# Kernel tuning notes

Hardware: AMD Instinct MI355X
Metric: run time of the kernel (lower is better)

The kernel has to match this reference:

```python
import jax, jax.numpy as jnp
import numpy as np

B, T, H, C = 256, 784, 512, 10
TRUNC = 100


def setup_inputs() -> dict:
    key = jax.random.key(0)
    ks = jax.random.split(key, 11)
    s_in = 1.0  # xavier-ish scales
    def init(k, shape, fan_in):
        return jax.random.normal(k, shape, dtype=jnp.float32) * (1.0 / np.sqrt(fan_in))
    return {
        "x": jax.random.normal(ks[0], (B, T), dtype=jnp.float32),
        "W_ih1": init(ks[1], (4 * H, 1), 1),
        "W_hh1": init(ks[2], (4 * H, H), H),
        "b_ih1": jnp.zeros((4 * H,), dtype=jnp.float32),
        "b_hh1": jnp.zeros((4 * H,), dtype=jnp.float32),
        "W_ih2": init(ks[3], (4 * H, H), H),
        "W_hh2": init(ks[4], (4 * H, H), H),
        "b_ih2": jnp.zeros((4 * H,), dtype=jnp.float32),
        "b_hh2": jnp.zeros((4 * H,), dtype=jnp.float32),
        "W_fc": init(ks[5], (C, H), H),
        "b_fc": jnp.zeros((C,), dtype=jnp.float32),
    }


def _lstm_cell(pre, h, c, W_hh, b_hh):
    # pre: input projection [B,4H]; PyTorch LSTMCell gate order: i, f, g, o
    gates = pre + h @ W_hh.T + b_hh
    i, f, g, o = jnp.split(gates, 4, axis=-1)
    c_new = jax.nn.sigmoid(f) * c + jax.nn.sigmoid(i) * jnp.tanh(g)
    h_new = jax.nn.sigmoid(o) * jnp.tanh(c_new)
    return h_new, c_new


def _forward(x, W_ih1, W_hh1, b_ih1, b_hh1, W_ih2, W_hh2, b_ih2, b_hh2, W_fc, b_fc):
    # Precompute input projections for layer 1 across all timesteps: x is scalar per step.
    # pre1_all: [T, B, 4H]
    pre1_all = x.T[:, :, None] * W_ih1[:, 0][None, None, :] + b_ih1
    t_idx = jnp.arange(T)

    def step(carry, xs):
        h1, c1, h2, c2 = carry
        pre1, t = xs
        # truncation point (detach) is identity in forward; kept for structure
        stop = (t % TRUNC) == 0
        sg = lambda a: jnp.where(stop, jax.lax.stop_gradient(a), a)
        h1, c1, h2, c2 = sg(h1), sg(c1), sg(h2), sg(c2)
        h1, c1 = _lstm_cell(pre1, h1, c1, W_hh1, b_hh1)
        pre2 = c1 @ W_ih2.T + b_ih2  # layer 2 consumes layer-1 CELL state
        h2, c2 = _lstm_cell(pre2, h2, c2, W_hh2, b_hh2)
        return (h1, c1, h2, c2), h2

    z = jnp.zeros((B, H), dtype=x.dtype)
    _, outs = jax.lax.scan(step, (z, z, z, z), (pre1_all, t_idx))  # outs: [T,B,H]
    outs = outs.transpose(1, 0, 2)  # [B,T,H]
    out = outs @ W_fc.T + b_fc  # [B,T,C]
    return out


def reference(x, W_ih1, W_hh1, b_ih1, b_hh1, W_ih2, W_hh2, b_ih2, b_hh2, W_fc, b_fc):
    return _forward(x, W_ih1, W_hh1, b_ih1, b_hh1, W_ih2, W_hh2, b_ih2, b_hh2, W_fc, b_fc)
```

## Files before the change

### kernel.cpp

```cpp
#include <hip/hip_runtime.h>


constexpr int Bn = 256;
constexpr int Tn = 784;
constexpr int Hn = 512;
constexpr int Cn = 10;

typedef short s16x8 __attribute__((ext_vector_type(8)));
typedef float f32x4 __attribute__((ext_vector_type(4)));

__device__ __forceinline__ unsigned short f2bf(float f) {
  unsigned u = __float_as_uint(f);
  u += 0x7FFFu + ((u >> 16) & 1u);
  return (unsigned short)(u >> 16);
}
__device__ __forceinline__ float bf2f(unsigned short s) {
  return __uint_as_float(((unsigned)s) << 16);
}
__device__ __forceinline__ float sigm(float v) { return 1.f / (1.f + __expf(-v)); }
__device__ __forceinline__ float tanh_(float v) {
  float vc = fminf(fmaxf(v, -15.f), 15.f);
  float e = __expf(2.f * vc);
  return (e - 1.f) / (e + 1.f);
}

__device__ __forceinline__ s16x8 load16_l2(const unsigned short* p) {
  s16x8 r;
  asm volatile("global_load_dwordx4 %0, %1, off sc0"
               : "=v"(r) : "v"(p) : "memory");
  return r;
}
__device__ __forceinline__ void store2_l2(unsigned short* p, unsigned short v) {
  unsigned w = v;
  asm volatile("global_store_short %0, %1, off"
               :: "v"(p), "v"(w) : "memory");
}
__device__ __forceinline__ void vm0_fence() {
  asm volatile("s_waitcnt vmcnt(0)" ::: "memory");
  __builtin_amdgcn_sched_barrier(0);
}
__device__ __forceinline__ unsigned ld_flag(const unsigned* p) {
  unsigned r;
  asm volatile("global_load_dword %0, %1, off sc0 sc1\n\ts_waitcnt vmcnt(0)"
               : "=v"(r) : "v"(p) : "memory");
  return r;
}

__device__ __forceinline__ void stage_w(char* smem, const float* W0,
                                        int js, int tid, int base) {
  for (int idx = tid * 4; idx < 64 * 512; idx += 1024) {
    int row = idx >> 9, kk = idx & 511;
    int n = ((row >> 4) << 9) + js + (row & 15);
    float4 w = *(const float4*)(W0 + (size_t)n * Hn + kk);
    short4 v = { (short)f2bf(w.x), (short)f2bf(w.y), (short)f2bf(w.z), (short)f2bf(w.w) };
    int byte = base + (row << 10) + ((((kk >> 3) ^ (row & 7)) << 4)) + ((kk & 7) << 1);
    *(short4*)(smem + byte) = v;
  }
}

__global__ void __launch_bounds__(256, 1)
lstm2_kernel(const float* __restrict__ x,
             const float* __restrict__ W_ih1, const float* __restrict__ W_hh1,
             const float* __restrict__ b_ih1, const float* __restrict__ b_hh1,
             const float* __restrict__ W_ih2, const float* __restrict__ W_hh2,
             const float* __restrict__ b_ih2, const float* __restrict__ b_hh2,
             const float* __restrict__ W_fc, const float* __restrict__ b_fc,
             float* __restrict__ out,
             unsigned* __restrict__ cnts,
             unsigned short* __restrict__ h1b,
             unsigned short* __restrict__ c1b,
             unsigned short* __restrict__ h2b)
{
  extern __shared__ char smem[];
  const int tid = threadIdx.x;
  const int wv = tid >> 6;
  const int l = tid & 63;

  if (tid == 0) {
    unsigned xcc;
    asm volatile("s_getreg_b32 %0, hwreg(HW_REG_XCC_ID)" : "=s"(xcc));
    xcc &= 7u;
    unsigned rk = atomicAdd(&cnts[512 + xcc * 16], 1u);
    *(unsigned*)(smem + 131064) = xcc;
    *(unsigned*)(smem + 131060) = rk;
  }
  __syncthreads();
  const int s8   = (int)*(const unsigned*)(smem + 131064);
  const int rank = (int)(*(const unsigned*)(smem + 131060) & 31u);
  const int rb = s8 << 5;
  const int js = rank << 4;
  unsigned* cnt = cnts + s8 * 64;

  const int rA = l & 15, lg = l >> 4, lx = l & 7;
  const bool isW1 = (wv < 2);

  s16x8 bw[64];
  stage_w(smem, W_hh1, js, tid, 0);
  __syncthreads();
  if (isW1) {
#pragma unroll
    for (int g = 0; g < 4; ++g)
#pragma unroll
      for (int kc = 0; kc < 16; ++kc)
        bw[(g << 4) + kc] =
            *(const s16x8*)(smem + (((g << 4) + rA) << 10) + ((((kc << 2) + lg) ^ lx) << 4));
  }
  __syncthreads();
  stage_w(smem, W_hh2, js, tid, 0);
  __syncthreads();
  if (!isW1) {
#pragma unroll
    for (int g = 0; g < 4; ++g)
#pragma unroll
      for (int kc = 0; kc < 16; ++kc)
        bw[(g << 4) + kc] =
            *(const s16x8*)(smem + (((g << 4) + rA) << 10) + ((((kc << 2) + lg) ^ lx) << 4));
  }
  __syncthreads();
  stage_w(smem, W_ih2, js, tid, 0);
  {
    unsigned short* wf = (unsigned short*)(smem + 65536);
    for (int idx = tid; idx < Cn * Hn; idx += 256) wf[idx] = f2bf(W_fc[idx]);
    if (tid < Cn) ((float*)(smem + 65536 + Cn * Hn * 2))[tid] = b_fc[tid];
  }
  __syncthreads();

  float wih1g[4], bg[4];
  {
    int col = js + rA;
#pragma unroll
    for (int g = 0; g < 4; ++g) {
      int n = (g << 9) + col;
      if (isW1) { wih1g[g] = W_ih1[n]; bg[g] = b_ih1[n] + b_hh1[n]; }
      else      { wih1g[g] = 0.f;      bg[g] = b_ih2[n] + b_hh2[n]; }
    }
  }

  const int rf = isW1 ? wv : (wv - 2);
  const int arow  = rb + (rf << 4) + rA;
  const int myrow = rb + (rf << 4) + (lg << 2);
  const int colj = js + rA;
  const int bfc = rb + rank;
  const int cg = wv * 5;

  const size_t SLAB = (size_t)Bn * Hn;
  float cst[4] = {0.f, 0.f, 0.f, 0.f};

  for (int k = 0; k <= Tn + 1; ++k) {
    if (tid == 0 && k > 0) {
      int g = 0;
      for (;;) {
        unsigned a = ld_flag(cnt);
        if ((int)a >= (k << 5)) break;
        if (++g > (1 << 20)) break;
        __builtin_amdgcn_s_sleep(1);
      }
    }
    __syncthreads();

    s16x8 h8;
    if (isW1 && k >= 2)
      h8 = load16_l2(h2b + (size_t)(k & 1) * SLAB + (size_t)bfc * Hn + (l << 3));

    if (isW1) {
      if (k < Tn) {
        float xv[4];
#pragma unroll
        for (int r = 0; r < 4; ++r) xv[r] = x[(size_t)(myrow + r) * Tn + k];
        s16x8 af[16];
        const unsigned short* Ab =
            h1b + (size_t)((k - 1) & 1) * SLAB + (size_t)arow * Hn + (lg << 3);
#pragma unroll
        for (int kc = 0; kc < 16; ++kc) af[kc] = load16_l2(Ab + kc * 32);
        vm0_fence();
        f32x4 acc[4];
#pragma unroll
        for (int g = 0; g < 4; ++g) acc[g] = f32x4{0.f, 0.f, 0.f, 0.f};
#pragma unroll
        for (int kc = 0; kc < 16; ++kc)
#pragma unroll
          for (int g = 0; g < 4; ++g)
            acc[g] = __builtin_amdgcn_mfma_f32_16x16x32_bf16(af[kc], bw[(g << 4) + kc], acc[g], 0, 0, 0);
        unsigned short* h1w = h1b + (size_t)(k & 1) * SLAB;
        unsigned short* c1w = c1b + (size_t)(k & 1) * SLAB;
#pragma unroll
        for (int r = 0; r < 4; ++r) {
          float iv = sigm(acc[0][r] + xv[r] * wih1g[0] + bg[0]);
          float ff = sigm(acc[1][r] + xv[r] * wih1g[1] + bg[1]);
          float gv = tanh_(acc[2][r] + xv[r] * wih1g[2] + bg[2]);
          float ov = sigm(acc[3][r] + xv[r] * wih1g[3] + bg[3]);
          float c = ff * cst[r] + iv * gv;
          cst[r] = c;
          float h = ov * tanh_(c);
          size_t off = (size_t)(myrow + r) * Hn + colj;
          store2_l2(h1w + off, f2bf(h));
          store2_l2(c1w + off, f2bf(c));
        }
      }
    } else {
      if (k >= 1 && k <= Tn) {
        const int t = k - 1;
        s16x8 af[16], cf[16];
        const unsigned short* Ab =
            h2b + (size_t)((t - 1) & 1) * SLAB + (size_t)arow * Hn + (lg << 3);
        const unsigned short* Cb =
            c1b + (size_t)(t & 1) * SLAB + (size_t)arow * Hn + (lg << 3);
#pragma unroll
        for (int kc = 0; kc < 16; ++kc) af[kc] = load16_l2(Ab + kc * 32);
#pragma unroll
        for (int kc = 0; kc < 16; ++kc) cf[kc] = load16_l2(Cb + kc * 32);
        vm0_fence();
        f32x4 acc[4];
#pragma unroll
        for (int g = 0; g < 4; ++g) acc[g] = f32x4{0.f, 0.f, 0.f, 0.f};
#pragma unroll
        for (int kc = 0; kc < 16; ++kc)
#pragma unroll
          for (int g = 0; g < 4; ++g)
            acc[g] = __builtin_amdgcn_mfma_f32_16x16x32_bf16(af[kc], bw[(g << 4) + kc], acc[g], 0, 0, 0);
#pragma unroll
        for (int kc = 0; kc < 16; ++kc)
#pragma unroll
          for (int g = 0; g < 4; ++g) {
            int byte = (((g << 4) + rA) << 10) + ((((kc << 2) + lg) ^ lx) << 4);
            acc[g] = __builtin_amdgcn_mfma_f32_16x16x32_bf16(cf[kc], *(const s16x8*)(smem + byte), acc[g], 0, 0, 0);
          }
        unsigned short* h2w = h2b + (size_t)(t & 1) * SLAB;
#pragma unroll
        for (int r = 0; r < 4; ++r) {
          float iv = sigm(acc[0][r] + bg[0]);
          float ff = sigm(acc[1][r] + bg[1]);
          float gv = tanh_(acc[2][r] + bg[2]);
          float ov = sigm(acc[3][r] + bg[3]);
          float c = ff * cst[r] + iv * gv;
          cst[r] = c;
          float h = ov * tanh_(c);
          store2_l2(h2w + (size_t)(myrow + r) * Hn + colj, f2bf(h));
        }
      }
    }

    vm0_fence();
    __syncthreads();
    if (tid == 0) atomicAdd(cnt, 1u);

    if (isW1 && k >= 2) {
      const unsigned short* wf = (const unsigned short*)(smem + 65536);
      float rs[5];
#pragma unroll
      for (int c5 = 0; c5 < 5; ++c5) {
        s16x8 w8 = *(const s16x8*)(wf + (size_t)(cg + c5) * Hn + (l << 3));
        float sum = 0.f;
#pragma unroll
        for (int i = 0; i < 8; ++i)
          sum += bf2f((unsigned short)h8[i]) * bf2f((unsigned short)w8[i]);
        rs[c5] = sum;
      }
#pragma unroll
      for (int c5 = 0; c5 < 5; ++c5) {
#pragma unroll
        for (int off = 32; off > 0; off >>= 1)
          rs[c5] += __shfl_xor(rs[c5], off);
      }
      if (l < 5) {
        float v = (l == 0) ? rs[0] : (l == 1) ? rs[1] : (l == 2) ? rs[2] : (l == 3) ? rs[3] : rs[4];
        v += ((const float*)(smem + 65536 + Cn * Hn * 2))[cg + l];
        out[(size_t)bfc * (Tn * Cn) + (size_t)(k - 2) * Cn + (cg + l)] = v;
      }
    }
  }
}

extern "C" void kernel_launch(void* const* d_in, const int* in_sizes, int n_in,
                              void* d_out, int out_size, void* d_ws, size_t ws_size,
                              hipStream_t stream) {
  const float* x     = (const float*)d_in[0];
  const float* W_ih1 = (const float*)d_in[1];
  const float* W_hh1 = (const float*)d_in[2];
  const float* b_ih1 = (const float*)d_in[3];
  const float* b_hh1 = (const float*)d_in[4];
  const float* W_ih2 = (const float*)d_in[5];
  const float* W_hh2 = (const float*)d_in[6];
  const float* b_ih2 = (const float*)d_in[7];
  const float* b_hh2 = (const float*)d_in[8];
  const float* W_fc  = (const float*)d_in[9];
  const float* b_fc  = (const float*)d_in[10];
  float* out = (float*)d_out;

  unsigned* cnts = (unsigned*)d_ws;
  unsigned short* h1b = (unsigned short*)((char*)d_ws + 4096);
  unsigned short* c1b = h1b + (size_t)2 * Bn * Hn;
  unsigned short* h2b = c1b + (size_t)2 * Bn * Hn;

  size_t zbytes = 4096 + (size_t)3 * 2 * Bn * Hn * sizeof(unsigned short);
  hipMemsetAsync(d_ws, 0, zbytes, stream);

  (void)hipFuncSetAttribute((const void*)lstm2_kernel,
                            hipFuncAttributeMaxDynamicSharedMemorySize, 131072);

  lstm2_kernel<<<dim3(256), dim3(256), 131072, stream>>>(
      x, W_ih1, W_hh1, b_ih1, b_hh1, W_ih2, W_hh2, b_ih2, b_hh2, W_fc, b_fc,
      out, cnts, h1b, c1b, h2b);
}
```

Baseline: 5.399 ms.

## Replace atomic step counter with per-block flags polled by a full wavefront

Each block now publishes its step number with a plain system-coherent store to its own flag slot instead of atomically incrementing a shared per-group counter. Wave 0 polls all 32 flags in parallel and uses a wave vote to detect completion. Separately, the per-fragment loads are merged into one inline-asm block of 16 immediate-offset loads, the four scalar stores are merged into one asm block with immediate offsets, and per-buffer base pointers are precomputed. The aim is to cut atomic contention and address arithmetic on the per-timestep critical path, at the cost of a wider workspace and a heavier polling wave.

```diff
diff --git a/kernel.cpp b/kernel.cpp
--- a/kernel.cpp
+++ b/kernel.cpp
@@ -30,20 +30,52 @@
                : "=v"(r) : "v"(p) : "memory");
   return r;
 }
-__device__ __forceinline__ void store2_l2(unsigned short* p, unsigned short v) {
-  unsigned w = v;
-  asm volatile("global_store_short %0, %1, off"
-               :: "v"(p), "v"(w) : "memory");
+__device__ __forceinline__ void load16x16_l2(const unsigned short* p, s16x8* f) {
+  asm volatile(
+      "global_load_dwordx4 %0, %16, off sc0\n\t"
+      "global_load_dwordx4 %1, %16, off offset:64 sc0\n\t"
+      "global_load_dwordx4 %2, %16, off offset:128 sc0\n\t"
+      "global_load_dwordx4 %3, %16, off offset:192 sc0\n\t"
+      "global_load_dwordx4 %4, %16, off offset:256 sc0\n\t"
+      "global_load_dwordx4 %5, %16, off offset:320 sc0\n\t"
+      "global_load_dwordx4 %6, %16, off offset:384 sc0\n\t"
+      "global_load_dwordx4 %7, %16, off offset:448 sc0\n\t"
+      "global_load_dwordx4 %8, %16, off offset:512 sc0\n\t"
+      "global_load_dwordx4 %9, %16, off offset:576 sc0\n\t"
+      "global_load_dwordx4 %10, %16, off offset:640 sc0\n\t"
+      "global_load_dwordx4 %11, %16, off offset:704 sc0\n\t"
+      "global_load_dwordx4 %12, %16, off offset:768 sc0\n\t"
+      "global_load_dwordx4 %13, %16, off offset:832 sc0\n\t"
+      "global_load_dwordx4 %14, %16, off offset:896 sc0\n\t"
+      "global_load_dwordx4 %15, %16, off offset:960 sc0"
+      : "=&v"(f[0]), "=&v"(f[1]), "=&v"(f[2]), "=&v"(f[3]),
+        "=&v"(f[4]), "=&v"(f[5]), "=&v"(f[6]), "=&v"(f[7]),
+        "=&v"(f[8]), "=&v"(f[9]), "=&v"(f[10]), "=&v"(f[11]),
+        "=&v"(f[12]), "=&v"(f[13]), "=&v"(f[14]), "=&v"(f[15])
+      : "v"(p) : "memory");
+}
+__device__ __forceinline__ void store4_l2(unsigned short* p, unsigned v0,
+                                          unsigned v1, unsigned v2, unsigned v3) {
+  asm volatile(
+      "global_store_short %0, %1, off\n\t"
+      "global_store_short %0, %2, off offset:1024\n\t"
+      "global_store_short %0, %3, off offset:2048\n\t"
+      "global_store_short %0, %4, off offset:3072"
+      :: "v"(p), "v"(v0), "v"(v1), "v"(v2), "v"(v3) : "memory");
 }
 __device__ __forceinline__ void vm0_fence() {
   asm volatile("s_waitcnt vmcnt(0)" ::: "memory");
   __builtin_amdgcn_sched_barrier(0);
 }
-__device__ __forceinline__ unsigned ld_flag(const unsigned* p) {
+__device__ __forceinline__ unsigned ld_flag_mall(const unsigned* p) {
   unsigned r;
   asm volatile("global_load_dword %0, %1, off sc0 sc1\n\ts_waitcnt vmcnt(0)"
                : "=v"(r) : "v"(p) : "memory");
   return r;
+}
+__device__ __forceinline__ void st_flag_mall(unsigned* p, unsigned v) {
+  asm volatile("global_store_dword %0, %1, off sc0 sc1"
+               :: "v"(p), "v"(v) : "memory");
 }
 
 __device__ __forceinline__ void stage_w(char* smem, const float* W0,
@@ -89,7 +121,9 @@
   const int rank = (int)(*(const unsigned*)(smem + 131060) & 31u);
   const int rb = s8 << 5;
   const int js = rank << 4;
-  unsigned* cnt = cnts + s8 * 64;
+
+  unsigned* fbase = cnts + 1024 + s8 * 32;
+  unsigned* myflag = fbase + rank;
 
   const int rA = l & 15, lg = l >> 4, lx = l & 7;
   const bool isW1 = (wv < 2);
@@ -144,14 +178,29 @@
   const int cg = wv * 5;
 
   const size_t SLAB = (size_t)Bn * Hn;
+  const size_t aoff = (size_t)arow * Hn + (lg << 3);
+  const unsigned short* h1A0 = h1b + aoff;
+  const unsigned short* h1A1 = h1b + SLAB + aoff;
+  const unsigned short* h2A0 = h2b + aoff;
+  const unsigned short* h2A1 = h2b + SLAB + aoff;
+  const unsigned short* c1A0 = c1b + aoff;
+  const unsigned short* c1A1 = c1b + SLAB + aoff;
+  const size_t woff = (size_t)myrow * Hn + colj;
+  unsigned short* h1W0 = h1b + woff;  unsigned short* h1W1 = h1b + SLAB + woff;
+  unsigned short* c1W0 = c1b + woff;  unsigned short* c1W1 = c1b + SLAB + woff;
+  unsigned short* h2W0 = h2b + woff;  unsigned short* h2W1 = h2b + SLAB + woff;
+  const unsigned short* fcA0 = h2b + (size_t)bfc * Hn + (l << 3);
+  const unsigned short* fcA1 = fcA0 + SLAB;
+
   float cst[4] = {0.f, 0.f, 0.f, 0.f};
 
   for (int k = 0; k <= Tn + 1; ++k) {
-    if (tid == 0 && k > 0) {
+    if (wv == 0 && k > 0) {
+      const unsigned* p = fbase + (l & 31);
       int g = 0;
       for (;;) {
-        unsigned a = ld_flag(cnt);
-        if ((int)a >= (k << 5)) break;
+        unsigned a = ld_flag_mall(p);
+        if (__all((int)a >= k)) break;
         if (++g > (1 << 20)) break;
         __builtin_amdgcn_s_sleep(1);
       }
@@ -160,7 +209,7 @@
 
     s16x8 h8;
     if (isW1 && k >= 2)
-      h8 = load16_l2(h2b + (size_t)(k & 1) * SLAB + (size_t)bfc * Hn + (l << 3));
+      h8 = load16_l2((k & 1) ? fcA1 : fcA0);
 
     if (isW1) {
       if (k < Tn) {
@@ -168,10 +217,7 @@
 #pragma unroll
         for (int r = 0; r < 4; ++r) xv[r] = x[(size_t)(myrow + r) * Tn + k];
         s16x8 af[16];
-        const unsigned short* Ab =
-            h1b + (size_t)((k - 1) & 1) * SLAB + (size_t)arow * Hn + (lg << 3);
-#pragma unroll
-        for (int kc = 0; kc < 16; ++kc) af[kc] = load16_l2(Ab + kc * 32);
+        load16x16_l2(((k - 1) & 1) ? h1A1 : h1A0, af);
         vm0_fence();
         f32x4 acc[4];
 #pragma unroll
@@ -181,8 +227,7 @@
 #pragma unroll
           for (int g = 0; g < 4; ++g)
             acc[g] = __builtin_amdgcn_mfma_f32_16x16x32_bf16(af[kc], bw[(g << 4) + kc], acc[g], 0, 0, 0);
-        unsigned short* h1w = h1b + (size_t)(k & 1) * SLAB;
-        unsigned short* c1w = c1b + (size_t)(k & 1) * SLAB;
+        unsigned hv[4], cv[4];
 #pragma unroll
         for (int r = 0; r < 4; ++r) {
           float iv = sigm(acc[0][r] + xv[r] * wih1g[0] + bg[0]);
@@ -191,24 +236,18 @@
           float ov = sigm(acc[3][r] + xv[r] * wih1g[3] + bg[3]);
           float c = ff * cst[r] + iv * gv;
           cst[r] = c;
-          float h = ov * tanh_(c);
-          size_t off = (size_t)(myrow + r) * Hn + colj;
-          store2_l2(h1w + off, f2bf(h));
-          store2_l2(c1w + off, f2bf(c));
+          hv[r] = f2bf(ov * tanh_(c));
+          cv[r] = f2bf(c);
         }
+        store4_l2((k & 1) ? h1W1 : h1W0, hv[0], hv[1], hv[2], hv[3]);
+        store4_l2((k & 1) ? c1W1 : c1W0, cv[0], cv[1], cv[2], cv[3]);
       }
     } else {
       if (k >= 1 && k <= Tn) {
         const int t = k - 1;
         s16x8 af[16], cf[16];
-        const unsigned short* Ab =
-            h2b + (size_t)((t - 1) & 1) * SLAB + (size_t)arow * Hn + (lg << 3);
-        const unsigned short* Cb =
-            c1b + (size_t)(t & 1) * SLAB + (size_t)arow * Hn + (lg << 3);
-#pragma unroll
-        for (int kc = 0; kc < 16; ++kc) af[kc] = load16_l2(Ab + kc * 32);
-#pragma unroll
-        for (int kc = 0; kc < 16; ++kc) cf[kc] = load16_l2(Cb + kc * 32);
+        load16x16_l2(((t - 1) & 1) ? h2A1 : h2A0, af);
+        load16x16_l2((t & 1) ? c1A1 : c1A0, cf);
         vm0_fence();
         f32x4 acc[4];
 #pragma unroll
@@ -225,7 +264,7 @@
             int byte = (((g << 4) + rA) << 10) + ((((kc << 2) + lg) ^ lx) << 4);
             acc[g] = __builtin_amdgcn_mfma_f32_16x16x32_bf16(cf[kc], *(const s16x8*)(smem + byte), acc[g], 0, 0, 0);
           }
-        unsigned short* h2w = h2b + (size_t)(t & 1) * SLAB;
+        unsigned hv[4];
 #pragma unroll
         for (int r = 0; r < 4; ++r) {
           float iv = sigm(acc[0][r] + bg[0]);
@@ -234,15 +273,15 @@
           float ov = sigm(acc[3][r] + bg[3]);
           float c = ff * cst[r] + iv * gv;
           cst[r] = c;
-          float h = ov * tanh_(c);
-          store2_l2(h2w + (size_t)(myrow + r) * Hn + colj, f2bf(h));
+          hv[r] = f2bf(ov * tanh_(c));
         }
+        store4_l2((t & 1) ? h2W1 : h2W0, hv[0], hv[1], hv[2], hv[3]);
       }
     }
 
     vm0_fence();
     __syncthreads();
-    if (tid == 0) atomicAdd(cnt, 1u);
+    if (tid == 0) st_flag_mall(myflag, (unsigned)(k + 1));
 
     if (isW1 && k >= 2) {
       const unsigned short* wf = (const unsigned short*)(smem + 65536);
@@ -288,11 +327,11 @@
   float* out = (float*)d_out;
 
   unsigned* cnts = (unsigned*)d_ws;
-  unsigned short* h1b = (unsigned short*)((char*)d_ws + 4096);
+  unsigned short* h1b = (unsigned short*)((char*)d_ws + 32768);
   unsigned short* c1b = h1b + (size_t)2 * Bn * Hn;
   unsigned short* h2b = c1b + (size_t)2 * Bn * Hn;
 
-  size_t zbytes = 4096 + (size_t)3 * 2 * Bn * Hn * sizeof(unsigned short);
+  size_t zbytes = 32768 + (size_t)3 * 2 * Bn * Hn * sizeof(unsigned short);
   hipMemsetAsync(d_ws, 0, zbytes, stream);
 
   (void)hipFuncSetAttribute((const void*)lstm2_kernel,
```

New measurement: 4.722 ms, median of 2. 12.5% less time.
